# Kernel tuning notes

Hardware: AMD Instinct MI355X
Metric: run time of the kernel (lower is better)

## Reference

```python
import jax, jax.numpy as jnp
import numpy as np

OUT, IN, BLK, RANK = 4096, 4096, 32, 16
N_BLOCKS = IN // BLK  # 128
Q_ZERO = 128.0  # center of unsigned code range, maps codes to signed values


def setup_inputs() -> dict:
    key = jax.random.key(0)
    ks = jax.random.split(key, 6)
    x = jax.random.normal(ks[0], (4, 2048, IN), dtype=jnp.float32)
    # GGML-style block-quantized weight: int codes in blocks of 32 + per-block fp scale
    q_weight = jax.random.randint(ks[1], (OUT, N_BLOCKS, BLK), 0, 256, dtype=jnp.int32)
    scales = jax.random.uniform(ks[2], (OUT, N_BLOCKS), dtype=jnp.float32) * 0.02
    # LoRA patch applied to dequantized weight
    lora_up = jax.random.normal(ks[3], (OUT, RANK), dtype=jnp.float32) * 0.02
    lora_down = jax.random.normal(ks[4], (RANK, IN), dtype=jnp.float32) * 0.02
    bias = jax.random.normal(ks[5], (OUT,), dtype=jnp.float32)
    return {"x": x, "q_weight": q_weight, "scales": scales,
            "lora_up": lora_up, "lora_down": lora_down, "bias": bias}


def reference(x, q_weight, scales, lora_up, lora_down, bias):
    # 1) dequantize: per-block scale * centered int codes -> full fp weight [OUT, IN]
    w = (q_weight.astype(jnp.float32) - Q_ZERO) * scales[:, :, None]
    w = w.reshape(OUT, IN)
    # 2) apply LoRA patch to the dequantized weight (patch function in get_weight)
    w = w + lora_up @ lora_down
    # 3) delegate to the linear forward operation: y = x @ W^T + b
    return jnp.einsum('bsd,od->bso', x, w) + bias
```

## Files before the change

### kernel.cpp

```cpp
#include <hip/hip_runtime.h>
#include <cstdint>
#include <cstddef>

#define M_TOT 8192
#define N_TOT 4096
#define K_TOT 4096
#define RANK  16

#define BM 256
#define BN 256
#define BK 64
#define NT (K_TOT / BK)

typedef float f32x4 __attribute__((ext_vector_type(4)));
typedef __bf16 bf16x8 __attribute__((ext_vector_type(8)));
typedef unsigned short u16x8 __attribute__((ext_vector_type(8)));

__device__ __forceinline__ unsigned short f32_to_bf16(float f) {
    union { float f; uint32_t u; } v; v.f = f;
    uint32_t r = v.u + (0x7fffu + ((v.u >> 16) & 1u));
    return (unsigned short)(r >> 16);
}

__device__ __forceinline__ void gload_lds16(const void* g, void* l) {
    __builtin_amdgcn_global_load_lds(
        (const __attribute__((address_space(1))) void*)g,
        (__attribute__((address_space(3))) void*)l,
        16, 0, 0);
}

__device__ __forceinline__ unsigned lds_addr(const void* p) {
    return (unsigned)(uintptr_t)(const __attribute__((address_space(3))) void*)p;
}

__device__ __forceinline__ bf16x8 dsr(unsigned addr) {
    bf16x8 r;
    asm volatile("ds_read_b128 %0, %1" : "=v"(r) : "v"(addr));
    return r;
}

__global__ __launch_bounds__(256) void convert_x_kernel(const float* __restrict__ x,
                                                        unsigned short* __restrict__ xb,
                                                        int n8) {
    int i = blockIdx.x * 256 + threadIdx.x;
    if (i >= n8) return;
    float4 a = ((const float4*)x)[2 * (size_t)i];
    float4 b = ((const float4*)x)[2 * (size_t)i + 1];
    u16x8 o;
    o[0] = f32_to_bf16(a.x); o[1] = f32_to_bf16(a.y);
    o[2] = f32_to_bf16(a.z); o[3] = f32_to_bf16(a.w);
    o[4] = f32_to_bf16(b.x); o[5] = f32_to_bf16(b.y);
    o[6] = f32_to_bf16(b.z); o[7] = f32_to_bf16(b.w);
    *(u16x8*)&xb[(size_t)i * 8] = o;
}

__global__ __launch_bounds__(256) void build_w_kernel(const int* __restrict__ q,
                                                      const float* __restrict__ scales,
                                                      const float* __restrict__ up,
                                                      const float* __restrict__ down,
                                                      unsigned short* __restrict__ W) {
    const int o0 = blockIdx.x * 4;
    const int t = threadIdx.x;
    __shared__ float u[4][RANK];
    if (t < 64) u[t >> 4][t & 15] = up[(o0 + (t >> 4)) * RANK + (t & 15)];
    __syncthreads();

#pragma unroll
    for (int cc = 0; cc < 2; cc++) {
        const int c = t + 256 * cc;
        const int k0 = c * 8;
        float acc[4][8];
#pragma unroll
        for (int row = 0; row < 4; row++) {
            const int o = o0 + row;
            int4 qa = *(const int4*)&q[(size_t)o * K_TOT + k0];
            int4 qb = *(const int4*)&q[(size_t)o * K_TOT + k0 + 4];
            const float s = scales[o * (K_TOT / 32) + (k0 >> 5)];
            acc[row][0] = (float)(qa.x - 128) * s;
            acc[row][1] = (float)(qa.y - 128) * s;
            acc[row][2] = (float)(qa.z - 128) * s;
            acc[row][3] = (float)(qa.w - 128) * s;
            acc[row][4] = (float)(qb.x - 128) * s;
            acc[row][5] = (float)(qb.y - 128) * s;
            acc[row][6] = (float)(qb.z - 128) * s;
            acc[row][7] = (float)(qb.w - 128) * s;
        }
#pragma unroll
        for (int r = 0; r < RANK; r++) {
            float4 da = *(const float4*)&down[r * K_TOT + k0];
            float4 db = *(const float4*)&down[r * K_TOT + k0 + 4];
#pragma unroll
            for (int row = 0; row < 4; row++) {
                const float ur = u[row][r];
                acc[row][0] += ur * da.x; acc[row][1] += ur * da.y;
                acc[row][2] += ur * da.z; acc[row][3] += ur * da.w;
                acc[row][4] += ur * db.x; acc[row][5] += ur * db.y;
                acc[row][6] += ur * db.z; acc[row][7] += ur * db.w;
            }
        }
#pragma unroll
        for (int row = 0; row < 4; row++) {
            u16x8 o8;
#pragma unroll
            for (int j = 0; j < 8; j++) o8[j] = f32_to_bf16(acc[row][j]);
            *(u16x8*)&W[(size_t)(o0 + row) * K_TOT + k0] = o8;
        }
    }
}

#define BARRIER() do { asm volatile("" ::: "memory"); \
                       __builtin_amdgcn_s_barrier(); \
                       asm volatile("" ::: "memory"); } while (0)
#define WAITL0()  asm volatile("s_waitcnt lgkmcnt(0)" ::: "memory")
#define VMCNT0()  asm volatile("s_waitcnt vmcnt(0)" ::: "memory")
#define SCHED0()  __builtin_amdgcn_sched_barrier(0)

__global__ __launch_bounds__(512, 2) void gemm_bt_kernel(const unsigned short* __restrict__ A,
                                                         const unsigned short* __restrict__ B,
                                                         const float* __restrict__ bias,
                                                         float* __restrict__ C) {
    __shared__ unsigned short As[2][2][128 * BK];
    __shared__ unsigned short Bs[2][2][128 * BK];

    const int tid  = (int)threadIdx.x;
    const int wave = tid >> 6;
    const int lane = tid & 63;
    const int wm   = wave >> 2;
    const int wn   = wave & 3;
    const int wbh  = wn >> 1;
    const int wbr  = (wn & 1) * 64;

    int lin = (int)(blockIdx.y * gridDim.x + blockIdx.x);
    lin = (lin & 7) * 64 + (lin >> 3);
    const int tile_n = (lin & 15) * BN;
    const int tile_m = (lin >> 4) * BM;

    const int srow  = tid >> 3;
    const int sk    = ((tid & 7) ^ (srow & 7)) * 8;
    const int wbase = wave * 512;

    const int l16  = lane & 15;
    const int quad = lane >> 4;
    const int sw   = l16 & 7;
    const int slot0 = ((quad ^ sw) * 8);
    const int slot1 = (((4 + quad) ^ sw) * 8);

    const unsigned short* aBase = A + (size_t)(tile_m + srow) * K_TOT + sk;
    const unsigned short* bBase = B + (size_t)(tile_n + srow) * K_TOT + sk;

#define STAGE_A(d, h, t) do { \
    gload_lds16(aBase + (size_t)((h) * 128) * K_TOT + (size_t)(t) * BK, &As[d][h][wbase]); \
    gload_lds16(aBase + (size_t)((h) * 128 + 64) * K_TOT + (size_t)(t) * BK, &As[d][h][4096 + wbase]); \
  } while (0)
#define STAGE_B(d, h, t) do { \
    gload_lds16(bBase + (size_t)((h) * 128) * K_TOT + (size_t)(t) * BK, &Bs[d][h][wbase]); \
    gload_lds16(bBase + (size_t)((h) * 128 + 64) * K_TOT + (size_t)(t) * BK, &Bs[d][h][4096 + wbase]); \
  } while (0)

    f32x4 acc[8][4];
#pragma unroll
    for (int i = 0; i < 8; i++)
#pragma unroll
        for (int j = 0; j < 4; j++) { f32x4 z = {0.f, 0.f, 0.f, 0.f}; acc[i][j] = z; }

    STAGE_A(0, 0, 0); STAGE_A(0, 1, 0);
    STAGE_B(0, 0, 0); STAGE_B(0, 1, 0);
    VMCNT0();
    BARRIER();

    for (int t = 0; t < NT; ++t) {
        const int cur = t & 1, nxt = cur ^ 1;

        const unsigned AhB = lds_addr(&As[cur][wm][l16 * BK]);
        const unsigned BhB = lds_addr(&Bs[cur][wbh][(wbr + l16) * BK]);
        const unsigned a0 = AhB + slot0 * 2, a1 = AhB + slot1 * 2;
        const unsigned b0 = BhB + slot0 * 2, b1 = BhB + slot1 * 2;

        bf16x8 bA[4], bB[4], aK[4];

#pragma unroll
        for (int ni = 0; ni < 4; ni++) bA[ni] = dsr(b0 + ni * 2048);
#pragma unroll
        for (int mi = 0; mi < 4; mi++) aK[mi] = dsr(a0 + mi * 2048);
        if (t + 1 < NT) STAGE_B(nxt, 0, t + 1);
        BARRIER();
        WAITL0();
        SCHED0();
        __builtin_amdgcn_s_setprio(1);
#pragma unroll
        for (int mi = 0; mi < 4; mi++)
#pragma unroll
            for (int ni = 0; ni < 4; ni++)
                acc[mi][ni] = __builtin_amdgcn_mfma_f32_16x16x32_bf16(aK[mi], bA[ni], acc[mi][ni], 0, 0, 0);
        __builtin_amdgcn_s_setprio(0);
        SCHED0();
        BARRIER();

#pragma unroll
        for (int ni = 0; ni < 4; ni++) bB[ni] = dsr(b1 + ni * 2048);
#pragma unroll
        for (int mi = 0; mi < 4; mi++) aK[mi] = dsr(a1 + mi * 2048);
        if (t + 1 < NT) STAGE_B(nxt, 1, t + 1);
        BARRIER();
        WAITL0();
        SCHED0();
        __builtin_amdgcn_s_setprio(1);
#pragma unroll
        for (int mi = 0; mi < 4; mi++)
#pragma unroll
            for (int ni = 0; ni < 4; ni++)
                acc[mi][ni] = __builtin_amdgcn_mfma_f32_16x16x32_bf16(aK[mi], bB[ni], acc[mi][ni], 0, 0, 0);
        __builtin_amdgcn_s_setprio(0);
        SCHED0();
        BARRIER();

#pragma unroll
        for (int mi = 0; mi < 4; mi++) aK[mi] = dsr(a0 + 8192 + mi * 2048);
        if (t + 1 < NT) { STAGE_A(nxt, 0, t + 1); STAGE_A(nxt, 1, t + 1); }
        BARRIER();
        WAITL0();
        SCHED0();
        __builtin_amdgcn_s_setprio(1);
#pragma unroll
        for (int mi = 0; mi < 4; mi++)
#pragma unroll
            for (int ni = 0; ni < 4; ni++)
                acc[mi + 4][ni] = __builtin_amdgcn_mfma_f32_16x16x32_bf16(aK[mi], bA[ni], acc[mi + 4][ni], 0, 0, 0);
        __builtin_amdgcn_s_setprio(0);
        SCHED0();
        BARRIER();

#pragma unroll
        for (int mi = 0; mi < 4; mi++) aK[mi] = dsr(a1 + 8192 + mi * 2048);
        BARRIER();
        WAITL0();
        SCHED0();
        __builtin_amdgcn_s_setprio(1);
#pragma unroll
        for (int mi = 0; mi < 4; mi++)
#pragma unroll
            for (int ni = 0; ni < 4; ni++)
                acc[mi + 4][ni] = __builtin_amdgcn_mfma_f32_16x16x32_bf16(aK[mi], bB[ni], acc[mi + 4][ni], 0, 0, 0);
        __builtin_amdgcn_s_setprio(0);
        SCHED0();
        VMCNT0();
        BARRIER();
    }

#pragma unroll
    for (int ni = 0; ni < 4; ni++) {
        const int col = tile_n + wn * 64 + ni * 16 + l16;
        const float bv = bias[col];
#pragma unroll
        for (int mi = 0; mi < 8; mi++) {
#pragma unroll
            for (int r = 0; r < 4; r++) {
                const int row = tile_m + wm * 128 + mi * 16 + quad * 4 + r;
                C[(size_t)row * N_TOT + col] = acc[mi][ni][r] + bv;
            }
        }
    }
#undef STAGE_A
#undef STAGE_B
}

extern "C" void kernel_launch(void* const* d_in, const int* in_sizes, int n_in,
                              void* d_out, int out_size, void* d_ws, size_t ws_size,
                              hipStream_t stream) {
    const float* x      = (const float*)d_in[0];
    const int*   q      = (const int*)d_in[1];
    const float* scales = (const float*)d_in[2];
    const float* up     = (const float*)d_in[3];
    const float* down   = (const float*)d_in[4];
    const float* bias   = (const float*)d_in[5];
    float* out = (float*)d_out;

    unsigned short* xb = (unsigned short*)d_ws;
    unsigned short* wb = xb + (size_t)M_TOT * K_TOT;

    const int n8 = M_TOT * K_TOT / 8;
    convert_x_kernel<<<n8 / 256, 256, 0, stream>>>(x, xb, n8);
    build_w_kernel<<<N_TOT / 4, 256, 0, stream>>>(q, scales, up, down, wb);
    gemm_bt_kernel<<<dim3(N_TOT / BN, M_TOT / BM), 512, 0, stream>>>(xb, wb, bias, out);
}
```

Before: 542.4 us.

## Hoist global prefetch and replace per-phase barriers with partial lgkmcnt waits

Issues all global-to-LDS staging for the next K tile at the start of each iteration, rather than spreading it across the four MFMA phases. It then reads all LDS fragments for the tile up front into separate register sets. The three intra-iteration barriers are replaced by graded lgkmcnt waits (8, 8, 4, 0), so each MFMA group waits only on the LDS reads it needs. This cuts synchronization stalls and overlaps LDS reads with MFMA work, at the cost of many more live fragment registers, which risks spills or lower occupancy.

```diff
diff --git a/kernel.cpp b/kernel.cpp
--- a/kernel.cpp
+++ b/kernel.cpp
@@ -111,7 +111,9 @@
 #define BARRIER() do { asm volatile("" ::: "memory"); \
                        __builtin_amdgcn_s_barrier(); \
                        asm volatile("" ::: "memory"); } while (0)
-#define WAITL0()  asm volatile("s_waitcnt lgkmcnt(0)" ::: "memory")
+#define WAITLG8() asm volatile("s_waitcnt lgkmcnt(8)" ::: "memory")
+#define WAITLG4() asm volatile("s_waitcnt lgkmcnt(4)" ::: "memory")
+#define WAITLG0() asm volatile("s_waitcnt lgkmcnt(0)" ::: "memory")
 #define VMCNT0()  asm volatile("s_waitcnt vmcnt(0)" ::: "memory")
 #define SCHED0()  __builtin_amdgcn_sched_barrier(0)
 
@@ -171,78 +173,76 @@
     for (int t = 0; t < NT; ++t) {
         const int cur = t & 1, nxt = cur ^ 1;
 
+        if (t + 1 < NT) {
+            STAGE_B(nxt, 0, t + 1); STAGE_B(nxt, 1, t + 1);
+            STAGE_A(nxt, 0, t + 1); STAGE_A(nxt, 1, t + 1);
+        }
+
         const unsigned AhB = lds_addr(&As[cur][wm][l16 * BK]);
         const unsigned BhB = lds_addr(&Bs[cur][wbh][(wbr + l16) * BK]);
         const unsigned a0 = AhB + slot0 * 2, a1 = AhB + slot1 * 2;
         const unsigned b0 = BhB + slot0 * 2, b1 = BhB + slot1 * 2;
 
-        bf16x8 bA[4], bB[4], aK[4];
-
-#pragma unroll
-        for (int ni = 0; ni < 4; ni++) bA[ni] = dsr(b0 + ni * 2048);
-#pragma unroll
-        for (int mi = 0; mi < 4; mi++) aK[mi] = dsr(a0 + mi * 2048);
-        if (t + 1 < NT) STAGE_B(nxt, 0, t + 1);
-        BARRIER();
-        WAITL0();
-        SCHED0();
-        __builtin_amdgcn_s_setprio(1);
-#pragma unroll
-        for (int mi = 0; mi < 4; mi++)
-#pragma unroll
-            for (int ni = 0; ni < 4; ni++)
-                acc[mi][ni] = __builtin_amdgcn_mfma_f32_16x16x32_bf16(aK[mi], bA[ni], acc[mi][ni], 0, 0, 0);
-        __builtin_amdgcn_s_setprio(0);
-        SCHED0();
-        BARRIER();
-
-#pragma unroll
-        for (int ni = 0; ni < 4; ni++) bB[ni] = dsr(b1 + ni * 2048);
-#pragma unroll
-        for (int mi = 0; mi < 4; mi++) aK[mi] = dsr(a1 + mi * 2048);
-        if (t + 1 < NT) STAGE_B(nxt, 1, t + 1);
-        BARRIER();
-        WAITL0();
-        SCHED0();
-        __builtin_amdgcn_s_setprio(1);
-#pragma unroll
-        for (int mi = 0; mi < 4; mi++)
-#pragma unroll
-            for (int ni = 0; ni < 4; ni++)
-                acc[mi][ni] = __builtin_amdgcn_mfma_f32_16x16x32_bf16(aK[mi], bB[ni], acc[mi][ni], 0, 0, 0);
-        __builtin_amdgcn_s_setprio(0);
-        SCHED0();
-        BARRIER();
-
-#pragma unroll
-        for (int mi = 0; mi < 4; mi++) aK[mi] = dsr(a0 + 8192 + mi * 2048);
-        if (t + 1 < NT) { STAGE_A(nxt, 0, t + 1); STAGE_A(nxt, 1, t + 1); }
-        BARRIER();
-        WAITL0();
-        SCHED0();
-        __builtin_amdgcn_s_setprio(1);
-#pragma unroll
-        for (int mi = 0; mi < 4; mi++)
-#pragma unroll
-            for (int ni = 0; ni < 4; ni++)
-                acc[mi + 4][ni] = __builtin_amdgcn_mfma_f32_16x16x32_bf16(aK[mi], bA[ni], acc[mi + 4][ni], 0, 0, 0);
-        __builtin_amdgcn_s_setprio(0);
-        SCHED0();
-        BARRIER();
-
-#pragma unroll
-        for (int mi = 0; mi < 4; mi++) aK[mi] = dsr(a1 + 8192 + mi * 2048);
-        BARRIER();
-        WAITL0();
-        SCHED0();
-        __builtin_amdgcn_s_setprio(1);
-#pragma unroll
-        for (int mi = 0; mi < 4; mi++)
-#pragma unroll
-            for (int ni = 0; ni < 4; ni++)
-                acc[mi + 4][ni] = __builtin_amdgcn_mfma_f32_16x16x32_bf16(aK[mi], bB[ni], acc[mi + 4][ni], 0, 0, 0);
-        __builtin_amdgcn_s_setprio(0);
-        SCHED0();
+        bf16x8 bA[4], bB[4], aK0[4], aK1[4], aH0[4], aH1[4];
+
+#pragma unroll
+        for (int ni = 0; ni < 4; ni++) bA[ni]  = dsr(b0 + ni * 2048);
+#pragma unroll
+        for (int mi = 0; mi < 4; mi++) aK0[mi] = dsr(a0 + mi * 2048);
+#pragma unroll
+        for (int ni = 0; ni < 4; ni++) bB[ni]  = dsr(b1 + ni * 2048);
+#pragma unroll
+        for (int mi = 0; mi < 4; mi++) aK1[mi] = dsr(a1 + mi * 2048);
+
+        WAITLG8();
+        SCHED0();
+        __builtin_amdgcn_s_setprio(1);
+#pragma unroll
+        for (int mi = 0; mi < 4; mi++)
+#pragma unroll
+            for (int ni = 0; ni < 4; ni++)
+                acc[mi][ni] = __builtin_amdgcn_mfma_f32_16x16x32_bf16(aK0[mi], bA[ni], acc[mi][ni], 0, 0, 0);
+        __builtin_amdgcn_s_setprio(0);
+        SCHED0();
+
+#pragma unroll
+        for (int mi = 0; mi < 4; mi++) aH0[mi] = dsr(a0 + 8192 + mi * 2048);
+#pragma unroll
+        for (int mi = 0; mi < 4; mi++) aH1[mi] = dsr(a1 + 8192 + mi * 2048);
+
+        WAITLG8();
+        SCHED0();
+        __builtin_amdgcn_s_setprio(1);
+#pragma unroll
+        for (int mi = 0; mi < 4; mi++)
+#pragma unroll
+            for (int ni = 0; ni < 4; ni++)
+                acc[mi][ni] = __builtin_amdgcn_mfma_f32_16x16x32_bf16(aK1[mi], bB[ni], acc[mi][ni], 0, 0, 0);
+        __builtin_amdgcn_s_setprio(0);
+        SCHED0();
+
+        WAITLG4();
+        SCHED0();
+        __builtin_amdgcn_s_setprio(1);
+#pragma unroll
+        for (int mi = 0; mi < 4; mi++)
+#pragma unroll
+            for (int ni = 0; ni < 4; ni++)
+                acc[mi + 4][ni] = __builtin_amdgcn_mfma_f32_16x16x32_bf16(aH0[mi], bA[ni], acc[mi + 4][ni], 0, 0, 0);
+        __builtin_amdgcn_s_setprio(0);
+        SCHED0();
+
+        WAITLG0();
+        SCHED0();
+        __builtin_amdgcn_s_setprio(1);
+#pragma unroll
+        for (int mi = 0; mi < 4; mi++)
+#pragma unroll
+            for (int ni = 0; ni < 4; ni++)
+                acc[mi + 4][ni] = __builtin_amdgcn_mfma_f32_16x16x32_bf16(aH1[mi], bB[ni], acc[mi + 4][ni], 0, 0, 0);
+        __builtin_amdgcn_s_setprio(0);
+        SCHED0();
+
         VMCNT0();
         BARRIER();
     }
```

Result: faster. 527.6 us (-2.7%).
